# Optimization experiments

Measured on AMD Instinct MI355X. Metric: run time of the kernel, lower is better.

## Reference

```python
import jax, jax.numpy as jnp
import numpy as np

LEAKY_SLOPE = 0.25
EPS_COS = 1e-8
EPS_NORM = 1e-12


def cosine_dist(x):
    # 1 - cosine similarity, matching cosine_distance_torch
    w = jnp.linalg.norm(x, axis=1, keepdims=True)  # [n,1]
    return 1.0 - (x @ x.T) / jnp.maximum(w * w.T, EPS_COS)


def gen_adj(x, edge_per_node):
    # gen_tr_adj_mat: threshold = (edge_per_node*n)-th smallest pairwise cosine distance,
    # zero diagonal, symmetrize via elementwise max, add I, L1 row-normalize.
    n = x.shape[0]
    dist = cosine_dist(x)  # [n,n]
    k = edge_per_node * n
    param = jax.lax.stop_gradient(jnp.partition(dist.ravel(), k)[k])
    eye = jnp.eye(n, dtype=x.dtype)
    g = (dist <= param).astype(x.dtype) * (1.0 - eye)
    adj = (1.0 - dist) * g
    adj_t = adj.T
    take_t = (adj_t > adj).astype(x.dtype)
    adj = adj + adj_t * take_t - adj * take_t  # elementwise max-symmetrize
    adj = adj + eye
    row_norm = jnp.maximum(jnp.sum(jnp.abs(adj), axis=1, keepdims=True), EPS_NORM)
    return adj / row_norm


def gcn_layer(x, adj, w, b):
    # dense mm -> (sparse) adj mm -> bias -> leaky_relu
    return jax.nn.leaky_relu(adj @ (x @ w) + b, LEAKY_SLOPE)


def setup_inputs() -> dict:
    key = jax.random.key(0)
    ks = jax.random.split(key, 8)
    n, d = 4000, 1000
    h = [400, 400, 200]
    x = jax.random.normal(ks[0], (n, d), jnp.float32)

    def xavier(k, fi, fo):
        std = (2.0 / (fi + fo)) ** 0.5
        return std * jax.random.normal(k, (fi, fo), jnp.float32)

    w1 = xavier(ks[1], d, h[0])
    w2 = xavier(ks[2], h[0], h[1])
    w3 = xavier(ks[3], h[1], h[2])
    b1 = jnp.zeros((h[0],), jnp.float32)
    b2 = jnp.zeros((h[1],), jnp.float32)
    b3 = jnp.zeros((h[2],), jnp.float32)
    adj_parameter = 10
    adj = gen_adj(x, adj_parameter)  # initial train adjacency, as in the pipeline
    return dict(adj_parameter=adj_parameter, x=x, adj=adj,
                w1=w1, b1=b1, w2=w2, b2=b2, w3=w3, b3=b3)


def reference(adj_parameter, x, adj, w1, b1, w2, b2, w3, b3):
    # eval mode: F.dropout(training=False) is identity
    x = gcn_layer(x, adj, w1, b1)
    adj = gen_adj(x, adj_parameter)
    x = gcn_layer(x, adj, w2, b2)
    adj = gen_adj(x, adj_parameter)
    x = gcn_layer(x, adj, w3, b3)
    return x
```

## Files before the change

### kernel.cpp

```cpp
#include <hip/hip_runtime.h>
#include <math.h>

#define NN 4000
#define KC 384
#define LEAKY 0.25f
#define HBLK 1000
#define NPART1 2016


template<int EPI>
__device__ inline float epi_apply(float v, int r, int c,
                                  const float* __restrict__ bias,
                                  const float* __restrict__ wn)
{
    if (EPI == 1) {
        float s = __fadd_rn(v, bias[c]);
        return (s >= 0.f) ? s : __fmul_rn(LEAKY, s);
    }
    if (EPI == 2) {
        float den = fmaxf(__fmul_rn(wn[r], wn[c]), 1e-8f);
        return __fsub_rn(1.0f, __fdiv_rn(v, den));
    }
    return v;
}

template<int XF>
__device__ float xf(float v)
{
    if (XF == 0) return __fmul_rn(v, v);
    return fabsf(v);
}

template<int XF>
__device__ float np_pairwise(const float* a, int n)
{
    if (n < 8) {
        float r = 0.f;
        for (int i = 0; i < n; ++i) r = __fadd_rn(r, xf<XF>(a[i]));
        return r;
    }
    if (n <= 128) {
        float r[8];
#pragma unroll
        for (int j = 0; j < 8; ++j) r[j] = xf<XF>(a[j]);
        int i = 8;
        const int lim = n - (n & 7);
        for (; i < lim; i += 8)
#pragma unroll
            for (int j = 0; j < 8; ++j) r[j] = __fadd_rn(r[j], xf<XF>(a[i + j]));
        float res = __fadd_rn(__fadd_rn(__fadd_rn(r[0], r[1]), __fadd_rn(r[2], r[3])),
                              __fadd_rn(__fadd_rn(r[4], r[5]), __fadd_rn(r[6], r[7])));
        for (; i < n; ++i) res = __fadd_rn(res, xf<XF>(a[i]));
        return res;
    }
    int n2 = (n / 2) & ~7;
    return __fadd_rn(np_pairwise<XF>(a, n2), np_pairwise<XF>(a + n2, n - n2));
}

__global__ __launch_bounds__(256, 4)
void gemm_tri64_k(const float* __restrict__ A, float* __restrict__ C,
                  unsigned* __restrict__ partial, int n, int K,
                  const float* __restrict__ wn)
{
    __shared__ float As[16][68];
    __shared__ float Bs[16][68];
    __shared__ unsigned lh[2048];
    const int tid = threadIdx.x;
    const int tx = tid & 15, ty = tid >> 4;
    const int sub = tid & 7;
    const int nt = (n + 63) >> 6;
    int bi = 0, rem = blockIdx.x;
    while (rem >= nt - bi) { rem -= nt - bi; ++bi; }
    const int bm = bi * 64, bn = (bi + rem) * 64;
    const bool diag = (rem == 0);

    for (int i = tid; i < 2048; i += 256) lh[i] = 0;

    float blk[4][4] = {};
    float acc[4][4];
    bool first = true;

    for (int kb = 0; kb < K; kb += KC) {
        const int kend = (kb + KC < K) ? kb + KC : K;
        for (int k0 = kb; k0 < kend; k0 += 16) {
            {
                int row = tid >> 2, q = tid & 3;
                int gr = bm + row, gk = k0 + q * 4;
                float4 v = make_float4(0.f, 0.f, 0.f, 0.f);
                if (gr < n) {
                    if (gk + 3 < kend) {
                        v = *(const float4*)(A + (size_t)gr * K + gk);
                    } else {
                        float* vp = (float*)&v;
#pragma unroll
                        for (int e = 0; e < 4; ++e)
                            if (gk + e < kend) vp[e] = A[(size_t)gr * K + gk + e];
                    }
                }
                float* vp = (float*)&v;
#pragma unroll
                for (int e = 0; e < 4; ++e) As[q * 4 + e][row] = vp[e];
            }
            {
                int row = tid >> 2, q = tid & 3;
                int gc = bn + row, gk = k0 + q * 4;
                float4 v = make_float4(0.f, 0.f, 0.f, 0.f);
                if (gc < n) {
                    if (gk + 3 < kend) {
                        v = *(const float4*)(A + (size_t)gc * K + gk);
                    } else {
                        float* vp = (float*)&v;
#pragma unroll
                        for (int e = 0; e < 4; ++e)
                            if (gk + e < kend) vp[e] = A[(size_t)gc * K + gk + e];
                    }
                }
                float* vp = (float*)&v;
#pragma unroll
                for (int e = 0; e < 4; ++e) Bs[q * 4 + e][row] = vp[e];
            }
            __syncthreads();
#pragma unroll
            for (int kk = 0; kk < 16; ++kk) {
                float a[4], b[4];
                *(float4*)&a[0] = *(const float4*)&As[kk][ty * 4];
                *(float4*)&b[0] = *(const float4*)&Bs[kk][tx * 4];
#pragma unroll
                for (int i = 0; i < 4; ++i)
#pragma unroll
                    for (int j = 0; j < 4; ++j)
                        blk[i][j] = fmaf(a[i], b[j], blk[i][j]);
            }
            __syncthreads();
        }
        if (first) {
#pragma unroll
            for (int i = 0; i < 4; ++i)
#pragma unroll
                for (int j = 0; j < 4; ++j) { acc[i][j] = blk[i][j]; blk[i][j] = 0.f; }
            first = false;
        } else {
#pragma unroll
            for (int i = 0; i < 4; ++i)
#pragma unroll
                for (int j = 0; j < 4; ++j) {
                    acc[i][j] = __fadd_rn(acc[i][j], blk[i][j]);
                    blk[i][j] = 0.f;
                }
        }
    }

#pragma unroll
    for (int i = 0; i < 4; ++i) {
        int r = bm + ty * 4 + i;
        if (r >= n) continue;
        float* Crow = C + (size_t)r * n;
        int c = bn + tx * 4;
        float v[4];
#pragma unroll
        for (int e = 0; e < 4; ++e)
            v[e] = epi_apply<2>(acc[i][e], r, c + e, nullptr, wn);
        if (c + 3 < n) {
            float4 s; s.x = v[0]; s.y = v[1]; s.z = v[2]; s.w = v[3];
            *(float4*)(Crow + c) = s;
        } else {
#pragma unroll
            for (int e = 0; e < 4; ++e)
                if (c + e < n) Crow[c + e] = v[e];
        }
#pragma unroll
        for (int e = 0; e < 4; ++e) {
            int cc = c + e;
            if (cc >= n) continue;
            unsigned w = 2u;
            if (diag) {
                if (cc < r) continue;
                if (cc == r) w = 1u;
            }
            unsigned u = __float_as_uint(v[e]);
            unsigned key = (u & 0x80000000u) ? ~u : (u | 0x80000000u);
            atomicAdd(&lh[(((key >> 24) & 0xFFu) << 3) | sub], w);
        }
    }
    __syncthreads();
    unsigned t = 0;
#pragma unroll
    for (int s = 0; s < 8; ++s) t += lh[(tid << 3) | s];
    partial[blockIdx.x * 256 + tid] = t;
}

template<int EPI>
__global__ __launch_bounds__(256, 4)
void gemm_s_k(const float* __restrict__ A, const float* __restrict__ B,
              float* __restrict__ C, int M, int N, int K,
              const float* __restrict__ bias)
{
    __shared__ float As[16][68];
    __shared__ float Bs[16][68];
    const int tid = threadIdx.x;
    const int tx = tid & 15, ty = tid >> 4;
    const int bm = blockIdx.y * 64, bn = blockIdx.x * 64;

    float blk[4][4] = {};
    float acc[4][4];
    bool first = true;

    for (int kb = 0; kb < K; kb += KC) {
        const int kend = (kb + KC < K) ? kb + KC : K;
        for (int k0 = kb; k0 < kend; k0 += 16) {
            {
                int row = tid >> 2, q = tid & 3;
                int gr = bm + row, gk = k0 + q * 4;
                float4 v = make_float4(0.f, 0.f, 0.f, 0.f);
                if (gr < M) {
                    if (gk + 3 < kend) {
                        v = *(const float4*)(A + (size_t)gr * K + gk);
                    } else {
                        float* vp = (float*)&v;
#pragma unroll
                        for (int e = 0; e < 4; ++e)
                            if (gk + e < kend) vp[e] = A[(size_t)gr * K + gk + e];
                    }
                }
                float* vp = (float*)&v;
#pragma unroll
                for (int e = 0; e < 4; ++e) As[q * 4 + e][row] = vp[e];
            }
            {
                int kk = tid >> 4, c = (tid & 15) * 4;
                int gk = k0 + kk, gc = bn + c;
                float4 v = make_float4(0.f, 0.f, 0.f, 0.f);
                if (gk < kend) {
                    if (gc + 3 < N) {
                        v = *(const float4*)(B + (size_t)gk * N + gc);
                    } else {
                        float* vp = (float*)&v;
#pragma unroll
                        for (int e = 0; e < 4; ++e)
                            if (gc + e < N) vp[e] = B[(size_t)gk * N + gc + e];
                    }
                }
                *(float4*)&Bs[kk][c] = v;
            }
            __syncthreads();
#pragma unroll
            for (int kk = 0; kk < 16; ++kk) {
                float a[4], b[4];
                *(float4*)&a[0] = *(const float4*)&As[kk][ty * 4];
                *(float4*)&b[0] = *(const float4*)&Bs[kk][tx * 4];
#pragma unroll
                for (int i = 0; i < 4; ++i)
#pragma unroll
                    for (int j = 0; j < 4; ++j)
                        blk[i][j] = fmaf(a[i], b[j], blk[i][j]);
            }
            __syncthreads();
        }
        if (first) {
#pragma unroll
            for (int i = 0; i < 4; ++i)
#pragma unroll
                for (int j = 0; j < 4; ++j) { acc[i][j] = blk[i][j]; blk[i][j] = 0.f; }
            first = false;
        } else {
#pragma unroll
            for (int i = 0; i < 4; ++i)
#pragma unroll
                for (int j = 0; j < 4; ++j) {
                    acc[i][j] = __fadd_rn(acc[i][j], blk[i][j]);
                    blk[i][j] = 0.f;
                }
        }
    }

#pragma unroll
    for (int i = 0; i < 4; ++i) {
        int r = bm + ty * 4 + i;
        if (r >= M) continue;
        float* Crow = C + (size_t)r * N;
        int c = bn + tx * 4;
        float v[4];
#pragma unroll
        for (int e = 0; e < 4; ++e)
            v[e] = epi_apply<EPI>(acc[i][e], r, c + e, bias, nullptr);
        if (c + 3 < N) {
            float4 s; s.x = v[0]; s.y = v[1]; s.z = v[2]; s.w = v[3];
            *(float4*)(Crow + c) = s;
        } else {
#pragma unroll
            for (int e = 0; e < 4; ++e)
                if (c + e < N) Crow[c + e] = v[e];
        }
    }
}

__global__ __launch_bounds__(256, 4)
void gemm_panel_k(const float* __restrict__ A, const float* __restrict__ B,
                  float* __restrict__ P, int M, int N, int K)
{
    __shared__ float As[16][68];
    __shared__ float Bs[16][68];
    const int tid = threadIdx.x;
    const int tx = tid & 15, ty = tid >> 4;
    const int bm = blockIdx.y * 64, bn = blockIdx.x * 64;
    const int kb = blockIdx.z * KC;
    const int kend = (kb + KC < K) ? kb + KC : K;
    float* Pp = P + (size_t)blockIdx.z * M * N;

    float blk[4][4] = {};

    for (int k0 = kb; k0 < kend; k0 += 16) {
        {
            int row = tid >> 2, q = tid & 3;
            int gr = bm + row, gk = k0 + q * 4;
            float4 v = make_float4(0.f, 0.f, 0.f, 0.f);
            if (gr < M) {
                if (gk + 3 < kend) {
                    v = *(const float4*)(A + (size_t)gr * K + gk);
                } else {
                    float* vp = (float*)&v;
#pragma unroll
                    for (int e = 0; e < 4; ++e)
                        if (gk + e < kend) vp[e] = A[(size_t)gr * K + gk + e];
                }
            }
            float* vp = (float*)&v;
#pragma unroll
            for (int e = 0; e < 4; ++e) As[q * 4 + e][row] = vp[e];
        }
        {
            int kk = tid >> 4, c = (tid & 15) * 4;
            int gk = k0 + kk, gc = bn + c;
            float4 v = make_float4(0.f, 0.f, 0.f, 0.f);
            if (gk < kend) {
                if (gc + 3 < N) {
                    v = *(const float4*)(B + (size_t)gk * N + gc);
                } else {
                    float* vp = (float*)&v;
#pragma unroll
                    for (int e = 0; e < 4; ++e)
                        if (gc + e < N) vp[e] = B[(size_t)gk * N + gc + e];
                }
            }
            *(float4*)&Bs[kk][c] = v;
        }
        __syncthreads();
#pragma unroll
        for (int kk = 0; kk < 16; ++kk) {
            float a[4], b[4];
            *(float4*)&a[0] = *(const float4*)&As[kk][ty * 4];
            *(float4*)&b[0] = *(const float4*)&Bs[kk][tx * 4];
#pragma unroll
            for (int i = 0; i < 4; ++i)
#pragma unroll
                for (int j = 0; j < 4; ++j)
                    blk[i][j] = fmaf(a[i], b[j], blk[i][j]);
        }
        __syncthreads();
    }

#pragma unroll
    for (int i = 0; i < 4; ++i) {
        int r = bm + ty * 4 + i;
        if (r >= M) continue;
        float* Prow = Pp + (size_t)r * N;
        int c = bn + tx * 4;
        if (c + 3 < N) {
            float4 s; s.x = blk[i][0]; s.y = blk[i][1];
            s.z = blk[i][2]; s.w = blk[i][3];
            *(float4*)(Prow + c) = s;
        } else {
#pragma unroll
            for (int e = 0; e < 4; ++e)
                if (c + e < N) Prow[c + e] = blk[i][e];
        }
    }
}

__global__ __launch_bounds__(256)
void combine3_k(const float* __restrict__ P, float* __restrict__ C, size_t nelem)
{
    const size_t i4 = (size_t)(blockIdx.x * 256 + threadIdx.x);
    const size_t stride = (size_t)gridDim.x * 256;
    const size_t n4 = nelem / 4;
    for (size_t i = i4; i < n4; i += stride) {
        float4 a = *(const float4*)(P + i * 4);
        float4 b = *(const float4*)(P + nelem + i * 4);
        float4 c = *(const float4*)(P + 2 * nelem + i * 4);
        float4 o;
        o.x = __fadd_rn(__fadd_rn(a.x, b.x), c.x);
        o.y = __fadd_rn(__fadd_rn(a.y, b.y), c.y);
        o.z = __fadd_rn(__fadd_rn(a.z, b.z), c.z);
        o.w = __fadd_rn(__fadd_rn(a.w, b.w), c.w);
        *(float4*)(C + i * 4) = o;
    }
}

__global__ __launch_bounds__(256)
void rownorm2_k(const float* __restrict__ X, float* __restrict__ wn)
{
    __shared__ float buf[400];
    __shared__ float leaf[4];
    const int row = blockIdx.x;
    const float* Xr = X + (size_t)row * 400;
    for (int i = threadIdx.x; i < 100; i += 256)
        *(float4*)&buf[i * 4] = *(const float4*)(Xr + i * 4);
    __syncthreads();
    if (threadIdx.x < 4) {
        const int off = (threadIdx.x >> 1) * 200 + ((threadIdx.x & 1) ? 96 : 0);
        const int len = (threadIdx.x & 1) ? 104 : 96;
        leaf[threadIdx.x] = np_pairwise<0>(buf + off, len);
    }
    __syncthreads();
    if (threadIdx.x == 0) {
        float s = __fadd_rn(__fadd_rn(leaf[0], leaf[1]),
                            __fadd_rn(leaf[2], leaf[3]));
        wn[row] = __fsqrt_rn(s);
    }
}

__global__ __launch_bounds__(256)
void rowabs2_k(const float* __restrict__ A, float* __restrict__ rs)
{
    __shared__ float buf[4000];
    __shared__ float leaf[8];
    const int row = blockIdx.x;
    const float* Ar = A + (size_t)row * 4000;
    for (int i = threadIdx.x; i < 1000; i += 256)
        *(float4*)&buf[i * 4] = *(const float4*)(Ar + i * 4);
    __syncthreads();
    if (threadIdx.x < 8) {
        const int off = (threadIdx.x >> 1) * 1000 + ((threadIdx.x & 1) ? 496 : 0);
        const int len = (threadIdx.x & 1) ? 504 : 496;
        leaf[threadIdx.x] = np_pairwise<1>(buf + off, len);
    }
    __syncthreads();
    if (threadIdx.x == 0) {
        float s = __fadd_rn(
            __fadd_rn(__fadd_rn(leaf[0], leaf[1]), __fadd_rn(leaf[2], leaf[3])),
            __fadd_rn(__fadd_rn(leaf[4], leaf[5]), __fadd_rn(leaf[6], leaf[7])));
        rs[row] = fmaxf(s, 1e-12f);
    }
}

__global__ void init_k(unsigned* __restrict__ state, const void* __restrict__ epn,
                       int* __restrict__ cnt)
{
    const int t = blockIdx.x * 256 + threadIdx.x;
    if (t < NN) cnt[t] = 0;
    if (t == 0) {
        int k = ((const int*)epn)[0];
        if (k <= 0 || k > 4000) {
            float f = ((const float*)epn)[0];
            if (f > 0.f && f <= 4000.f) k = (int)f;
            else {
                long long ll = ((const long long*)epn)[0];
                if (ll > 0 && ll <= 4000) k = (int)ll;
                else {
                    double dd = ((const double*)epn)[0];
                    k = (dd > 0.0 && dd <= 4000.0) ? (int)dd : 10;
                }
            }
        }
        state[0] = 0u;
        state[1] = (unsigned)(k * NN);
    }
}

__global__ __launch_bounds__(256)
void hist_tri_k(const float* __restrict__ dist, unsigned* __restrict__ partial,
                const unsigned* __restrict__ state, int shift, int n)
{
    __shared__ unsigned lh[2048];
    for (int i = threadIdx.x; i < 2048; i += 256) lh[i] = 0;
    __syncthreads();
    const unsigned prefix = state[0];
    const int sub = threadIdx.x & 7;
    const int npair = (n + 1) / 2;
    for (int p = blockIdx.x; p < npair; p += HBLK) {
#pragma unroll
        for (int half = 0; half < 2; ++half) {
            const int i = half ? (n - 1 - p) : p;
            if (half && i == p) break;
            const float* row = dist + (size_t)i * n;
            for (int j = i + threadIdx.x; j < n; j += 256) {
                unsigned u = __float_as_uint(row[j]);
                unsigned key = (u & 0x80000000u) ? ~u : (u | 0x80000000u);
                bool ok = ((key >> (shift + 8)) == prefix);
                if (ok) atomicAdd(&lh[((((key >> shift) & 0xFFu)) << 3) | sub],
                                  (j == i) ? 1u : 2u);
            }
        }
    }
    __syncthreads();
    unsigned t = 0;
#pragma unroll
    for (int s = 0; s < 8; ++s) t += lh[(threadIdx.x << 3) | s];
    partial[blockIdx.x * 256 + threadIdx.x] = t;
}

__global__ __launch_bounds__(256)
void reduce_k(const unsigned* __restrict__ partial, int nparts,
              unsigned* __restrict__ hist256)
{
    const int bin = blockIdx.x;
    const int tid = threadIdx.x;
    unsigned s = 0;
    for (int i = tid; i < nparts; i += 256)
        s += partial[(size_t)i * 256 + bin];
    __shared__ unsigned sh[256];
    sh[tid] = s;
    __syncthreads();
    for (int off = 128; off > 0; off >>= 1) {
        if (tid < off) sh[tid] += sh[tid + off];
        __syncthreads();
    }
    if (tid == 0) hist256[bin] = sh[0];
}

__global__ __launch_bounds__(256)
void scan256_k(const unsigned* __restrict__ hist256, unsigned* __restrict__ state,
               int shift, float* __restrict__ param)
{
    const int tid = threadIdx.x;
    unsigned h = hist256[tid];
    __shared__ unsigned sh[256];
    sh[tid] = h;
    __syncthreads();
    for (int off = 1; off < 256; off <<= 1) {
        unsigned v = (tid >= off) ? sh[tid - off] : 0;
        __syncthreads();
        sh[tid] += v;
        __syncthreads();
    }
    const unsigned incl = sh[tid], excl = incl - h;
    const unsigned krem = state[1];
    if (krem >= excl && krem < incl) {
        unsigned np = (state[0] << 8) | (unsigned)tid;
        state[0] = np;
        state[1] = krem - excl;
        if (shift == 0) {
            unsigned u = (np & 0x80000000u) ? (np ^ 0x80000000u) : ~np;
            *param = __uint_as_float(u);
        }
    }
}

__device__ inline float thr_f(float d, int i, int j, float p)
{
    float a = (d <= p && i != j) ? __fsub_rn(1.0f, d) : 0.0f;
    return (i == j) ? 1.0f : a;
}

__global__ __launch_bounds__(256)
void symthresh_mirror_k(float* __restrict__ adj, const float* __restrict__ param,
                        int* __restrict__ cnt, int n)
{
    __shared__ float TB[64][65];
    const float p = *param;
    const int nt = (n + 63) >> 6;
    int bi = 0, rem = blockIdx.x;
    while (rem >= nt - bi) { rem -= nt - bi; ++bi; }
    const int bj = bi + rem;
    const int tid = threadIdx.x;
    const int lane = tid & 63;
    const int r0i = bi * 64, r0j = bj * 64;

#pragma unroll
    for (int it = 0; it < 16; ++it) {
        int idx = tid + it * 256;
        int q = idx >> 6, c = idx & 63;
        int gr = r0i + q, gc = r0j + c;
        bool inb = (gr < n && gc < n);
        float a = 0.f;
        if (inb) {
            a = thr_f(adj[(size_t)gr * n + gc], gr, gc, p);
            adj[(size_t)gr * n + gc] = a;
            TB[q][c] = a;
        }
        unsigned long long m = __ballot(inb && a != 0.0f);
        if (lane == 0 && gr < n) atomicAdd(&cnt[gr], (int)__popcll(m));
    }
    __syncthreads();
    if (bi != bj) {
#pragma unroll
        for (int it = 0; it < 16; ++it) {
            int idx = tid + it * 256;
            int q = idx >> 6, c = idx & 63;
            int gr = r0j + q, gc = r0i + c;
            bool inb = (gr < n && gc < n);
            float a = 0.f;
            if (inb) {
                a = TB[c][q];
                adj[(size_t)gr * n + gc] = a;
            }
            unsigned long long m = __ballot(inb && a != 0.0f);
            if (lane == 0 && gr < n) atomicAdd(&cnt[gr], (int)__popcll(m));
        }
    }
}

__global__ __launch_bounds__(256)
void norm_k(float* __restrict__ adj, const float* __restrict__ rs, int n)
{
    const int i = blockIdx.y;
    const int j = blockIdx.x * 256 + threadIdx.x;
    if (j >= n) return;
    const size_t idx = (size_t)i * n + j;
    adj[idx] = __fdiv_rn(adj[idx], rs[i]);
}

__global__ __launch_bounds__(256)
void count_k(const float* __restrict__ A, int* __restrict__ cnt, int n)
{
    const int gw = (blockIdx.x * blockDim.x + threadIdx.x) >> 6;
    if (gw >= n) return;
    const int lane = threadIdx.x & 63;
    int c = 0;
    for (int k0 = 0; k0 < n; k0 += 64) {
        int k = k0 + lane;
        bool nz = (k < n) && (A[(size_t)gw * n + k] != 0.0f);
        unsigned long long m = __ballot(nz);
        c += (int)__popcll(m);
    }
    if (lane == 0) cnt[gw] = c;
}

__global__ __launch_bounds__(1024)
void scanrows_k(const int* __restrict__ cnt, int* __restrict__ roff)
{
    const int t = threadIdx.x;
    int vals[4];
    int s0 = 0;
#pragma unroll
    for (int e = 0; e < 4; ++e) {
        int r = t * 4 + e;
        vals[e] = (r < NN) ? cnt[r] : 0;
        s0 += vals[e];
    }
    __shared__ int sh[1024];
    sh[t] = s0;
    __syncthreads();
    for (int off = 1; off < 1024; off <<= 1) {
        int v = (t >= off) ? sh[t - off] : 0;
        __syncthreads();
        sh[t] += v;
        __syncthreads();
    }
    int excl = sh[t] - s0;
#pragma unroll
    for (int e = 0; e < 4; ++e) {
        int r = t * 4 + e;
        if (r <= NN) roff[r] = excl;
        excl += vals[e];
    }
    if (t == 1023) roff[NN] = sh[1023];
}

template<bool DIV>
__global__ __launch_bounds__(256)
void fill_k(const float* __restrict__ A, const int* __restrict__ roff,
            const float* __restrict__ rs, int* __restrict__ ridx,
            float* __restrict__ rval, int n)
{
    const int gw = (blockIdx.x * blockDim.x + threadIdx.x) >> 6;
    if (gw >= n) return;
    const int lane = threadIdx.x & 63;
    const float r = DIV ? rs[gw] : 1.0f;
    int base = roff[gw];
    const unsigned long long ltmask = (lane == 63) ? ~0ULL >> 1
                                                   : ((1ULL << lane) - 1);
    for (int k0 = 0; k0 < n; k0 += 64) {
        int k = k0 + lane;
        float v = (k < n) ? A[(size_t)gw * n + k] : 0.f;
        bool nz = (v != 0.0f);
        unsigned long long m = __ballot(nz);
        if (nz) {
            int pos = base + (int)__popcll(m & ltmask);
            ridx[pos] = k;
            rval[pos] = DIV ? __fdiv_rn(v, r) : v;
        }
        base += (int)__popcll(m);
    }
}

template<bool WN>
__global__ __launch_bounds__(256)
void spmm_k(const int* __restrict__ roff, const int* __restrict__ ridx,
            const float* __restrict__ rval, const float* __restrict__ T,
            const float* __restrict__ bias, float* __restrict__ H, int ncols,
            float* __restrict__ wn)
{
    __shared__ int ks[128];
    __shared__ float vs[128];
    __shared__ float buf[512];
    __shared__ float leaf[4];
    const int r = blockIdx.x;
    const int tid = threadIdx.x;
    const int c0 = tid, c1 = tid + 256;
    const bool ok0 = c0 < ncols, ok1 = c1 < ncols;
    float acc0 = 0.f, blk0 = 0.f, acc1 = 0.f, blk1 = 0.f;
    int nb = KC;
    const int s = roff[r], e = roff[r + 1];
    for (int base = s; base < e; base += 128) {
        const int m = (e - base < 128) ? (e - base) : 128;
        __syncthreads();
        if (tid < m) { ks[tid] = ridx[base + tid]; vs[tid] = rval[base + tid]; }
        __syncthreads();
        for (int t = 0; t < m; ++t) {
            const int k = ks[t];
            const float v = vs[t];
            while (k >= nb) {
                acc0 = __fadd_rn(acc0, blk0); blk0 = 0.f;
                acc1 = __fadd_rn(acc1, blk1); blk1 = 0.f;
                nb += KC;
            }
            const float* Tr = T + (size_t)k * ncols;
            if (ok0) blk0 = fmaf(v, Tr[c0], blk0);
            if (ok1) blk1 = fmaf(v, Tr[c1], blk1);
        }
    }
    acc0 = __fadd_rn(acc0, blk0);
    acc1 = __fadd_rn(acc1, blk1);
    float h0 = 0.f, h1 = 0.f;
    if (ok0) {
        float s0 = __fadd_rn(acc0, bias[c0]);
        h0 = (s0 >= 0.f) ? s0 : __fmul_rn(LEAKY, s0);
        H[(size_t)r * ncols + c0] = h0;
    }
    if (ok1) {
        float s1 = __fadd_rn(acc1, bias[c1]);
        h1 = (s1 >= 0.f) ? s1 : __fmul_rn(LEAKY, s1);
        H[(size_t)r * ncols + c1] = h1;
    }
    if (WN) {
        if (ok0) buf[c0] = h0;
        if (ok1) buf[c1] = h1;
        __syncthreads();
        if (tid < 4) {
            const int off = (tid >> 1) * 200 + ((tid & 1) ? 96 : 0);
            const int len = (tid & 1) ? 104 : 96;
            leaf[tid] = np_pairwise<0>(buf + off, len);
        }
        __syncthreads();
        if (tid == 0) {
            float s2 = __fadd_rn(__fadd_rn(leaf[0], leaf[1]),
                                 __fadd_rn(leaf[2], leaf[3]));
            wn[r] = __fsqrt_rn(s2);
        }
    }
}

template<int EPI, bool TRANSB, bool FIRST, bool LAST>
__global__ __launch_bounds__(256, 4)
void gemm_pass_k(const float* __restrict__ A, const float* __restrict__ B,
                 float* __restrict__ C, int M, int N, int K, int kb, int kend,
                 const float* __restrict__ bias, const float* __restrict__ wn)
{
    __shared__ float As[16][132];
    __shared__ float Bs[16][132];
    const int tid = threadIdx.x;
    const int tx = tid & 15, ty = tid >> 4;
    const int bm = blockIdx.y * 128, bn = blockIdx.x * 128;

    float blk[8][8] = {};

    for (int k0 = kb; k0 < kend; k0 += 16) {
#pragma unroll
        for (int it = 0; it < 2; ++it) {
            int idx = tid + it * 256;
            int row = idx >> 2, q = idx & 3;
            int gr = bm + row, gk = k0 + q * 4;
            float4 v = make_float4(0.f, 0.f, 0.f, 0.f);
            if (gr < M) {
                if (gk + 3 < kend) {
                    v = *(const float4*)(A + (size_t)gr * K + gk);
                } else {
                    float* vp = (float*)&v;
#pragma unroll
                    for (int e = 0; e < 4; ++e)
                        if (gk + e < kend) vp[e] = A[(size_t)gr * K + gk + e];
                }
            }
            float* vp = (float*)&v;
#pragma unroll
            for (int e = 0; e < 4; ++e) As[q * 4 + e][row] = vp[e];
        }
        if (!TRANSB) {
#pragma unroll
            for (int it = 0; it < 2; ++it) {
                int idx = tid + it * 256;
                int kk = idx >> 5, cq = idx & 31;
                int gk = k0 + kk, c = cq * 4, gc = bn + c;
                float4 v = make_float4(0.f, 0.f, 0.f, 0.f);
                if (gk < kend) {
                    if (gc + 3 < N) {
                        v = *(const float4*)(B + (size_t)gk * N + gc);
                    } else {
                        float* vp = (float*)&v;
#pragma unroll
                        for (int e = 0; e < 4; ++e)
                            if (gc + e < N) vp[e] = B[(size_t)gk * N + gc + e];
                    }
                }
                *(float4*)&Bs[kk][c] = v;
            }
        } else {
#pragma unroll
            for (int it = 0; it < 2; ++it) {
                int idx = tid + it * 256;
                int row = idx >> 2, q = idx & 3;
                int gc = bn + row, gk = k0 + q * 4;
                float4 v = make_float4(0.f, 0.f, 0.f, 0.f);
                if (gc < N) {
                    if (gk + 3 < kend) {
                        v = *(const float4*)(B + (size_t)gc * K + gk);
                    } else {
                        float* vp = (float*)&v;
#pragma unroll
                        for (int e = 0; e < 4; ++e)
                            if (gk + e < kend) vp[e] = B[(size_t)gc * K + gk + e];
                    }
                }
                float* vp = (float*)&v;
#pragma unroll
                for (int e = 0; e < 4; ++e) Bs[q * 4 + e][row] = vp[e];
            }
        }
        __syncthreads();
#pragma unroll
        for (int kk = 0; kk < 16; ++kk) {
            float a[8], b[8];
            *(float4*)&a[0] = *(const float4*)&As[kk][ty * 4];
            *(float4*)&a[4] = *(const float4*)&As[kk][ty * 4 + 64];
            *(float4*)&b[0] = *(const float4*)&Bs[kk][tx * 4];
            *(float4*)&b[4] = *(const float4*)&Bs[kk][tx * 4 + 64];
#pragma unroll
            for (int i = 0; i < 8; ++i)
#pragma unroll
                for (int j = 0; j < 8; ++j)
                    blk[i][j] = fmaf(a[i], b[j], blk[i][j]);
        }
        __syncthreads();
    }

#pragma unroll
    for (int i = 0; i < 8; ++i) {
        int r = bm + ty * 4 + (i & 3) + (i >> 2) * 64;
        if (r >= M) continue;
        float* Crow = C + (size_t)r * N;
#pragma unroll
        for (int h = 0; h < 2; ++h) {
            int c = bn + tx * 4 + h * 64;
            float v[4];
#pragma unroll
            for (int e = 0; e < 4; ++e) v[e] = blk[i][h * 4 + e];
            if (c + 3 < N) {
                if (!FIRST) {
                    float4 o = *(const float4*)(Crow + c);
                    v[0] = __fadd_rn(o.x, v[0]); v[1] = __fadd_rn(o.y, v[1]);
                    v[2] = __fadd_rn(o.z, v[2]); v[3] = __fadd_rn(o.w, v[3]);
                }
                if (LAST) {
#pragma unroll
                    for (int e = 0; e < 4; ++e)
                        v[e] = epi_apply<EPI>(v[e], r, c + e, bias, wn);
                }
                float4 s; s.x = v[0]; s.y = v[1]; s.z = v[2]; s.w = v[3];
                *(float4*)(Crow + c) = s;
            } else {
#pragma unroll
                for (int e = 0; e < 4; ++e) {
                    if (c + e >= N) continue;
                    float vv = v[e];
                    if (!FIRST) vv = __fadd_rn(Crow[c + e], vv);
                    if (LAST) vv = epi_apply<EPI>(vv, r, c + e, bias, wn);
                    Crow[c + e] = vv;
                }
            }
        }
    }
}

template<int EPI, bool TRANSB>
static void run_gemm(const float* A, const float* B, float* C,
                     int M, int N, int K, const float* bias, const float* wn,
                     hipStream_t stream)
{
    const int nb = (K + KC - 1) / KC;
    const dim3 grid((N + 127) / 128, (M + 127) / 128);
    for (int p = 0; p < nb; ++p) {
        const int kb = p * KC;
        const int kend = (kb + KC < K) ? kb + KC : K;
        const bool first = (p == 0), last = (p == nb - 1);
        if (first && last)
            gemm_pass_k<EPI, TRANSB, true, true><<<grid, 256, 0, stream>>>(
                A, B, C, M, N, K, kb, kend, bias, wn);
        else if (first)
            gemm_pass_k<EPI, TRANSB, true, false><<<grid, 256, 0, stream>>>(
                A, B, C, M, N, K, kb, kend, bias, wn);
        else if (last)
            gemm_pass_k<EPI, TRANSB, false, true><<<grid, 256, 0, stream>>>(
                A, B, C, M, N, K, kb, kend, bias, wn);
        else
            gemm_pass_k<EPI, TRANSB, false, false><<<grid, 256, 0, stream>>>(
                A, B, C, M, N, K, kb, kend, bias, wn);
    }
}

extern "C" void kernel_launch(void* const* d_in, const int* in_sizes, int n_in,
                              void* d_out, int out_size, void* d_ws, size_t ws_size,
                              hipStream_t stream)
{
    const void*  epn  = d_in[0];
    const float* x    = (const float*)d_in[1];
    const float* adj0 = (const float*)d_in[2];
    const float* w1   = (const float*)d_in[3];
    const float* b1   = (const float*)d_in[4];
    const float* w2   = (const float*)d_in[5];
    const float* b2   = (const float*)d_in[6];
    const float* w3   = (const float*)d_in[7];
    const float* b3   = (const float*)d_in[8];
    float* out = (float*)d_out;

    char* ws = (char*)d_ws;
    float*    dist    = (float*)   ws;
    float*    Tbuf    = (float*)  (ws + 64000000);
    float*    H1      = (float*)  (ws + 70400000);
    float*    H2      = (float*)  (ws + 76800000);
    float*    wn      = (float*)  (ws + 83200000);
    float*    rs      = (float*)  (ws + 83216000);
    unsigned* state   = (unsigned*)(ws + 83232000);
    float*    param   = (float*)  (ws + 83232008);
    unsigned* hist256 = (unsigned*)(ws + 83232064);
    unsigned* partial = (unsigned*)(ws + 83233088);
    int*      cnt     = (int*)    (ws + 85297472);
    int*      roff    = (int*)    (ws + 85313472);
    int*      ridx    = (int*)    (ws + 85329480);
    float*    rval    = (float*)  (ws + 101329480);
    float*    panels  = (float*)  (ws + 85329480);
    const bool use_csr = (ws_size >= 117329480ULL + 64);

    const int gsN = (NN + 63) / 64;
    const int nt64 = (NN + 63) / 64;
    const int nsym64 = nt64 * (nt64 + 1) / 2;

    auto genadj = [&](const float* H, bool have_wn) {
        if (!have_wn)
            rownorm2_k<<<NN, 256, 0, stream>>>(H, wn);
        gemm_tri64_k<<<nsym64, 256, 0, stream>>>(H, dist, partial, NN, 400, wn);
        init_k<<<16, 256, 0, stream>>>(state, epn, cnt);
        reduce_k<<<256, 256, 0, stream>>>(partial, NPART1, hist256);
        scan256_k<<<1, 256, 0, stream>>>(hist256, state, 24, param);
        for (int p = 1; p < 4; ++p) {
            const int shift = 24 - 8 * p;
            hist_tri_k<<<HBLK, 256, 0, stream>>>(dist, partial, state, shift, NN);
            reduce_k<<<256, 256, 0, stream>>>(partial, HBLK, hist256);
            scan256_k<<<1, 256, 0, stream>>>(hist256, state, shift, param);
        }
        symthresh_mirror_k<<<nsym64, 256, 0, stream>>>(dist, param, cnt, NN);
        rowabs2_k<<<NN, 256, 0, stream>>>(dist, rs);
    };

    auto aggregate_pre = [&](const float* Aadj, const float* Tm,
                             const float* bias, float* Hout, int ncols,
                             bool want_wn) {
        if (use_csr) {
            count_k<<<(NN + 3) / 4, 256, 0, stream>>>(Aadj, cnt, NN);
            scanrows_k<<<1, 1024, 0, stream>>>(cnt, roff);
            fill_k<false><<<(NN + 3) / 4, 256, 0, stream>>>(Aadj, roff, nullptr,
                                                            ridx, rval, NN);
            if (want_wn)
                spmm_k<true><<<NN, 256, 0, stream>>>(roff, ridx, rval, Tm, bias,
                                                     Hout, ncols, wn);
            else
                spmm_k<false><<<NN, 256, 0, stream>>>(roff, ridx, rval, Tm, bias,
                                                      Hout, ncols, nullptr);
        } else {
            run_gemm<1, false>(Aadj, Tm, Hout, NN, ncols, NN, bias,
                               nullptr, stream);
        }
    };

    auto aggregate_rs = [&](float* Aadj, const float* Tm,
                            const float* bias, float* Hout, int ncols,
                            bool want_wn) {
        if (use_csr) {
            scanrows_k<<<1, 1024, 0, stream>>>(cnt, roff);
            fill_k<true><<<(NN + 3) / 4, 256, 0, stream>>>(Aadj, roff, rs,
                                                           ridx, rval, NN);
            if (want_wn)
                spmm_k<true><<<NN, 256, 0, stream>>>(roff, ridx, rval, Tm, bias,
                                                     Hout, ncols, wn);
            else
                spmm_k<false><<<NN, 256, 0, stream>>>(roff, ridx, rval, Tm, bias,
                                                      Hout, ncols, nullptr);
        } else {
            norm_k<<<dim3((NN + 255) / 256, NN), 256, 0, stream>>>(Aadj, rs, NN);
            run_gemm<1, false>(Aadj, Tm, Hout, NN, ncols, NN, bias,
                               nullptr, stream);
        }
    };

    if (use_csr) {
        gemm_panel_k<<<dim3((400 + 63) / 64, gsN, 3), 256, 0, stream>>>(
            x, w1, panels, NN, 400, 1000);
        combine3_k<<<1024, 256, 0, stream>>>(panels, Tbuf, (size_t)NN * 400);
    } else {
        gemm_s_k<0><<<dim3((400 + 63) / 64, gsN), 256, 0, stream>>>(
            x, w1, Tbuf, NN, 400, 1000, nullptr);
    }
    aggregate_pre(adj0, Tbuf, b1, H1, 400, use_csr);

    genadj(H1, use_csr);
    gemm_s_k<0><<<dim3((400 + 63) / 64, gsN), 256, 0, stream>>>(
        H1, w2, Tbuf, NN, 400, 400, nullptr);
    aggregate_rs(dist, Tbuf, b2, H2, 400, use_csr);

    genadj(H2, use_csr);
    gemm_s_k<0><<<dim3((200 + 63) / 64, gsN), 256, 0, stream>>>(
        H2, w3, Tbuf, NN, 200, 400, nullptr);
    aggregate_rs(dist, Tbuf, b3, out, 200, false);
}
```

Measured before the change: 860.5 us.

## Double-buffer shared-memory tiles in both SGEMM kernels with register prefetch

Both the triangular cosine-distance GEMM and the generic GEMM now use two shared-memory buffers. The next K-tile is loaded into registers while the current tile is computed, then written to the other buffer, so each K step needs one barrier instead of two. The aim is to hide global-load latency behind the FMAs. In exchange it doubles the tile LDS, adds prefetch registers that may lower occupancy under launch_bounds(256,4), and rewrites the KC-chunked accumulation boundary logic.

```diff
diff --git a/kernel.cpp b/kernel.cpp
--- a/kernel.cpp
+++ b/kernel.cpp
@@ -62,8 +62,8 @@
                   unsigned* __restrict__ partial, int n, int K,
                   const float* __restrict__ wn)
 {
-    __shared__ float As[16][68];
-    __shared__ float Bs[16][68];
+    __shared__ float As[2][16][68];
+    __shared__ float Bs[2][16][68];
     __shared__ unsigned lh[2048];
     const int tid = threadIdx.x;
     const int tx = tid & 15, ty = tid >> 4;
@@ -76,78 +76,93 @@
 
     for (int i = tid; i < 2048; i += 256) lh[i] = 0;
 
+    const int srow = tid >> 2, sq = tid & 3;
+
+    auto load_tile = [&](int k0, float4& ra, float4& rb) {
+        int gk = k0 + sq * 4;
+        ra = make_float4(0.f, 0.f, 0.f, 0.f);
+        rb = make_float4(0.f, 0.f, 0.f, 0.f);
+        int gr = bm + srow;
+        if (gr < n) {
+            if (gk + 3 < K) {
+                ra = *(const float4*)(A + (size_t)gr * K + gk);
+            } else {
+                float* vp = (float*)&ra;
+#pragma unroll
+                for (int e = 0; e < 4; ++e)
+                    if (gk + e < K) vp[e] = A[(size_t)gr * K + gk + e];
+            }
+        }
+        int gc = bn + srow;
+        if (gc < n) {
+            if (gk + 3 < K) {
+                rb = *(const float4*)(A + (size_t)gc * K + gk);
+            } else {
+                float* vp = (float*)&rb;
+#pragma unroll
+                for (int e = 0; e < 4; ++e)
+                    if (gk + e < K) vp[e] = A[(size_t)gc * K + gk + e];
+            }
+        }
+    };
+    auto write_tile = [&](int buf, const float4& ra, const float4& rb) {
+        const float* ap = (const float*)&ra;
+        const float* bp = (const float*)&rb;
+#pragma unroll
+        for (int e = 0; e < 4; ++e) {
+            As[buf][sq * 4 + e][srow] = ap[e];
+            Bs[buf][sq * 4 + e][srow] = bp[e];
+        }
+    };
+
     float blk[4][4] = {};
     float acc[4][4];
     bool first = true;
 
-    for (int kb = 0; kb < K; kb += KC) {
-        const int kend = (kb + KC < K) ? kb + KC : K;
-        for (int k0 = kb; k0 < kend; k0 += 16) {
-            {
-                int row = tid >> 2, q = tid & 3;
-                int gr = bm + row, gk = k0 + q * 4;
-                float4 v = make_float4(0.f, 0.f, 0.f, 0.f);
-                if (gr < n) {
-                    if (gk + 3 < kend) {
-                        v = *(const float4*)(A + (size_t)gr * K + gk);
-                    } else {
-                        float* vp = (float*)&v;
-#pragma unroll
-                        for (int e = 0; e < 4; ++e)
-                            if (gk + e < kend) vp[e] = A[(size_t)gr * K + gk + e];
+    const int ntile = (K + 15) / 16;
+    {
+        float4 ra, rb;
+        load_tile(0, ra, rb);
+        write_tile(0, ra, rb);
+    }
+    __syncthreads();
+
+    for (int t = 0; t < ntile; ++t) {
+        const int cur = t & 1;
+        float4 na, nb;
+        const bool have_next = (t + 1 < ntile);
+        if (have_next) load_tile((t + 1) * 16, na, nb);
+#pragma unroll
+        for (int kk = 0; kk < 16; ++kk) {
+            float a[4], b[4];
+            *(float4*)&a[0] = *(const float4*)&As[cur][kk][ty * 4];
+            *(float4*)&b[0] = *(const float4*)&Bs[cur][kk][tx * 4];
+#pragma unroll
+            for (int i = 0; i < 4; ++i)
+#pragma unroll
+                for (int j = 0; j < 4; ++j)
+                    blk[i][j] = fmaf(a[i], b[j], blk[i][j]);
+        }
+        if (have_next) write_tile(cur ^ 1, na, nb);
+        const int knext = (t + 1) * 16;
+        if (knext % KC == 0 || knext >= K) {
+            if (first) {
+#pragma unroll
+                for (int i = 0; i < 4; ++i)
+#pragma unroll
+                    for (int j = 0; j < 4; ++j) { acc[i][j] = blk[i][j]; blk[i][j] = 0.f; }
+                first = false;
+            } else {
+#pragma unroll
+                for (int i = 0; i < 4; ++i)
+#pragma unroll
+                    for (int j = 0; j < 4; ++j) {
+                        acc[i][j] = __fadd_rn(acc[i][j], blk[i][j]);
+                        blk[i][j] = 0.f;
                     }
-                }
-                float* vp = (float*)&v;
-#pragma unroll
-                for (int e = 0; e < 4; ++e) As[q * 4 + e][row] = vp[e];
-            }
-            {
-                int row = tid >> 2, q = tid & 3;
-                int gc = bn + row, gk = k0 + q * 4;
-                float4 v = make_float4(0.f, 0.f, 0.f, 0.f);
-                if (gc < n) {
-                    if (gk + 3 < kend) {
-                        v = *(const float4*)(A + (size_t)gc * K + gk);
-                    } else {
-                        float* vp = (float*)&v;
-#pragma unroll
-                        for (int e = 0; e < 4; ++e)
-                            if (gk + e < kend) vp[e] = A[(size_t)gc * K + gk + e];
-                    }
-                }
-                float* vp = (float*)&v;
-#pragma unroll
-                for (int e = 0; e < 4; ++e) Bs[q * 4 + e][row] = vp[e];
-            }
-            __syncthreads();
-#pragma unroll
-            for (int kk = 0; kk < 16; ++kk) {
-                float a[4], b[4];
-                *(float4*)&a[0] = *(const float4*)&As[kk][ty * 4];
-                *(float4*)&b[0] = *(const float4*)&Bs[kk][tx * 4];
-#pragma unroll
-                for (int i = 0; i < 4; ++i)
-#pragma unroll
-                    for (int j = 0; j < 4; ++j)
-                        blk[i][j] = fmaf(a[i], b[j], blk[i][j]);
-            }
-            __syncthreads();
-        }
-        if (first) {
-#pragma unroll
-            for (int i = 0; i < 4; ++i)
-#pragma unroll
-                for (int j = 0; j < 4; ++j) { acc[i][j] = blk[i][j]; blk[i][j] = 0.f; }
-            first = false;
-        } else {
-#pragma unroll
-            for (int i = 0; i < 4; ++i)
-#pragma unroll
-                for (int j = 0; j < 4; ++j) {
-                    acc[i][j] = __fadd_rn(acc[i][j], blk[i][j]);
-                    blk[i][j] = 0.f;
-                }
-        }
+            }
+        }
+        __syncthreads();
     }
 
 #pragma unroll
@@ -183,10 +198,10 @@
         }
     }
     __syncthreads();
-    unsigned t = 0;
-#pragma unroll
-    for (int s = 0; s < 8; ++s) t += lh[(tid << 3) | s];
-    partial[blockIdx.x * 256 + tid] = t;
+    unsigned t2 = 0;
+#pragma unroll
+    for (int s = 0; s < 8; ++s) t2 += lh[(tid << 3) | s];
+    partial[blockIdx.x * 256 + tid] = t2;
 }
 
 template<int EPI>
@@ -195,82 +210,100 @@
               float* __restrict__ C, int M, int N, int K,
               const float* __restrict__ bias)
 {
-    __shared__ float As[16][68];
-    __shared__ float Bs[16][68];
+    __shared__ float As[2][16][68];
+    __shared__ float Bs[2][16][68];
     const int tid = threadIdx.x;
     const int tx = tid & 15, ty = tid >> 4;
     const int bm = blockIdx.y * 64, bn = blockIdx.x * 64;
 
+    const int arow = tid >> 2, aq = tid & 3;
+    const int bkk = tid >> 4, bc = (tid & 15) * 4;
+
+    auto load_tile = [&](int k0, float4& ra, float4& rb) {
+        ra = make_float4(0.f, 0.f, 0.f, 0.f);
+        rb = make_float4(0.f, 0.f, 0.f, 0.f);
+        {
+            int gr = bm + arow, gk = k0 + aq * 4;
+            if (gr < M) {
+                if (gk + 3 < K) {
+                    ra = *(const float4*)(A + (size_t)gr * K + gk);
+                } else {
+                    float* vp = (float*)&ra;
+#pragma unroll
+                    for (int e = 0; e < 4; ++e)
+                        if (gk + e < K) vp[e] = A[(size_t)gr * K + gk + e];
+                }
+            }
+        }
+        {
+            int gk = k0 + bkk, gc = bn + bc;
+            if (gk < K) {
+                if (gc + 3 < N) {
+                    rb = *(const float4*)(B + (size_t)gk * N + gc);
+                } else {
+                    float* vp = (float*)&rb;
+#pragma unroll
+                    for (int e = 0; e < 4; ++e)
+                        if (gc + e < N) vp[e] = B[(size_t)gk * N + gc + e];
+                }
+            }
+        }
+    };
+    auto write_tile = [&](int buf, const float4& ra, const float4& rb) {
+        const float* ap = (const float*)&ra;
+#pragma unroll
+        for (int e = 0; e < 4; ++e) As[buf][aq * 4 + e][arow] = ap[e];
+        *(float4*)&Bs[buf][bkk][bc] = rb;
+    };
+
     float blk[4][4] = {};
     float acc[4][4];
     bool first = true;
 
-    for (int kb = 0; kb < K; kb += KC) {
-        const int kend = (kb + KC < K) ? kb + KC : K;
-        for (int k0 = kb; k0 < kend; k0 += 16) {
-            {
-                int row = tid >> 2, q = tid & 3;
-                int gr = bm + row, gk = k0 + q * 4;
-                float4 v = make_float4(0.f, 0.f, 0.f, 0.f);
-                if (gr < M) {
-                    if (gk + 3 < kend) {
-                        v = *(const float4*)(A + (size_t)gr * K + gk);
-                    } else {
-                        float* vp = (float*)&v;
-#pragma unroll
-                        for (int e = 0; e < 4; ++e)
-                            if (gk + e < kend) vp[e] = A[(size_t)gr * K + gk + e];
+    const int ntile = (K + 15) / 16;
+    {
+        float4 ra, rb;
+        load_tile(0, ra, rb);
+        write_tile(0, ra, rb);
+    }
+    __syncthreads();
+
+    for (int t = 0; t < ntile; ++t) {
+        const int cur = t & 1;
+        float4 na, nb;
+        const bool have_next = (t + 1 < ntile);
+        if (have_next) load_tile((t + 1) * 16, na, nb);
+#pragma unroll
+        for (int kk = 0; kk < 16; ++kk) {
+            float a[4], b[4];
+            *(float4*)&a[0] = *(const float4*)&As[cur][kk][ty * 4];
+            *(float4*)&b[0] = *(const float4*)&Bs[cur][kk][tx * 4];
+#pragma unroll
+            for (int i = 0; i < 4; ++i)
+#pragma unroll
+                for (int j = 0; j < 4; ++j)
+                    blk[i][j] = fmaf(a[i], b[j], blk[i][j]);
+        }
+        if (have_next) write_tile(cur ^ 1, na, nb);
+        const int knext = (t + 1) * 16;
+        if (knext % KC == 0 || knext >= K) {
+            if (first) {
+#pragma unroll
+                for (int i = 0; i < 4; ++i)
+#pragma unroll
+                    for (int j = 0; j < 4; ++j) { acc[i][j] = blk[i][j]; blk[i][j] = 0.f; }
+                first = false;
+            } else {
+#pragma unroll
+                for (int i = 0; i < 4; ++i)
+#pragma unroll
+                    for (int j = 0; j < 4; ++j) {
+                        acc[i][j] = __fadd_rn(acc[i][j], blk[i][j]);
+                        blk[i][j] = 0.f;
                     }
-                }
-                float* vp = (float*)&v;
-#pragma unroll
-                for (int e = 0; e < 4; ++e) As[q * 4 + e][row] = vp[e];
-            }
-            {
-                int kk = tid >> 4, c = (tid & 15) * 4;
-                int gk = k0 + kk, gc = bn + c;
-                float4 v = make_float4(0.f, 0.f, 0.f, 0.f);
-                if (gk < kend) {
-                    if (gc + 3 < N) {
-                        v = *(const float4*)(B + (size_t)gk * N + gc);
-                    } else {
-                        float* vp = (float*)&v;
-#pragma unroll
-                        for (int e = 0; e < 4; ++e)
-                            if (gc + e < N) vp[e] = B[(size_t)gk * N + gc + e];
-                    }
-                }
-                *(float4*)&Bs[kk][c] = v;
-            }
-            __syncthreads();
-#pragma unroll
-            for (int kk = 0; kk < 16; ++kk) {
-                float a[4], b[4];
-                *(float4*)&a[0] = *(const float4*)&As[kk][ty * 4];
-                *(float4*)&b[0] = *(const float4*)&Bs[kk][tx * 4];
-#pragma unroll
-                for (int i = 0; i < 4; ++i)
-#pragma unroll
-                    for (int j = 0; j < 4; ++j)
-                        blk[i][j] = fmaf(a[i], b[j], blk[i][j]);
-            }
-            __syncthreads();
-        }
-        if (first) {
-#pragma unroll
-            for (int i = 0; i < 4; ++i)
-#pragma unroll
-                for (int j = 0; j < 4; ++j) { acc[i][j] = blk[i][j]; blk[i][j] = 0.f; }
-            first = false;
-        } else {
-#pragma unroll
-            for (int i = 0; i < 4; ++i)
-#pragma unroll
-                for (int j = 0; j < 4; ++j) {
-                    acc[i][j] = __fadd_rn(acc[i][j], blk[i][j]);
-                    blk[i][j] = 0.f;
-                }
-        }
+            }
+        }
+        __syncthreads();
     }
 
 #pragma unroll
```

Measured after the change: 2.350 ms. 2.73x slower.
